# Kernel optimization log

Hardware: AMD Instinct MI355X
Metric: run time of the kernel (lower is better)

## Reference

```python
import jax, jax.numpy as jnp
import numpy as np

EMBED_DIM = 768
MAX_LEN = 1024
ALPHA = 0.99
BATCH = 16


def setup_inputs() -> dict:
    key = jax.random.key(0)
    k1, k2, k3 = jax.random.split(key, 3)
    x = jax.random.normal(k1, (BATCH, MAX_LEN, EMBED_DIM), dtype=jnp.float32)
    # torch nn.Linear(embed_dim, 3*embed_dim): store weight as [in, out] for x @ W
    scale = 1.0 / np.sqrt(EMBED_DIM)
    W_qkv = jax.random.uniform(k2, (EMBED_DIM, 3 * EMBED_DIM), dtype=jnp.float32,
                               minval=-scale, maxval=scale)
    b_qkv = jax.random.uniform(k3, (3 * EMBED_DIM,), dtype=jnp.float32,
                               minval=-scale, maxval=scale)
    return {"x": x, "W_qkv": W_qkv, "b_qkv": b_qkv}


def _retention_mask(sl, alpha, dtype):
    # M[i, j] = alpha**(i - j) if i >= j else 0 (causal tril * decay)
    i = jnp.arange(sl)[:, None]
    j = jnp.arange(sl)[None, :]
    causal = i >= j
    # compute decay only where causal to avoid huge alpha**(negative) values
    exponent = jnp.where(causal, (i - j).astype(dtype), 0.0)
    decay = jnp.asarray(alpha, dtype) ** exponent
    return jnp.where(causal, decay, jnp.zeros((), dtype))


def reference(x, W_qkv, b_qkv):
    bs, sl, d = x.shape
    qkv = x @ W_qkv + b_qkv                      # [B, S, 3D]
    q, k, v = jnp.split(qkv, 3, axis=-1)         # each [B, S, D]
    M = _retention_mask(sl, ALPHA, x.dtype)      # [S, S]
    scores = jnp.einsum('bsd,btd->bst', q, k) / jnp.sqrt(jnp.asarray(d, x.dtype))
    out = jnp.einsum('bst,btd->bsd', scores * M[None, :, :], v)
    return out
```

## Files before the change

### kernel.cpp

```cpp
#include <hip/hip_runtime.h>
#include <hip/hip_bf16.h>


#define SEQ   1024
#define DIM   768
#define ND3   2304

typedef __attribute__((ext_vector_type(8))) short bf16x8;
typedef __attribute__((ext_vector_type(4))) float f32x4;

#define L2A     (-0.014499569695115089f)
#define RSQRTD  (0.03608439182435161f)

__device__ __forceinline__ unsigned short f2bf(float x) {
  union { float f; unsigned u; } v; v.f = x;
  unsigned r = v.u + 0x7FFFu + ((v.u >> 16) & 1u);
  return (unsigned short)(r >> 16);
}

__device__ __forceinline__ void gload16(const void* g, void* l) {
  __builtin_amdgcn_global_load_lds(
      (const __attribute__((address_space(1))) void*)g,
      (__attribute__((address_space(3))) void*)l, 16, 0, 0);
}

__device__ __forceinline__ void gemm256(
    const unsigned short* pA, const unsigned short* pB, int ldA, int ldB,
    char* ls, int nt, int wid, int lane, f32x4 acc[8][4]) {
  int lr = lane & 15, lg = lane >> 4;
  int wm = wid >> 2, wn = wid & 3;
  int slot16 = (((((lr & 1) << 2) | lg) ^ ((lr >> 1) & 7)) << 4);
  int rdA = wm * 8192 + (lr >> 1) * 128 + slot16;
  int rdB = 16384 + wn * 4096 + (lr >> 1) * 128 + slot16;
  int cc = wid * 2;

#define STG(t, half) do {                                                     \
    char* d_ = ls + ((t) & 3) * 32768 + (half) * 16384 + cc * 1024;           \
    const unsigned short* s_ = ((half) ? pB : pA) + (size_t)(t) * 32;         \
    int ld_ = ((half) ? ldB : ldA);                                           \
    gload16(s_ + (size_t)(cc * 16) * ld_, d_);                                \
    gload16(s_ + (size_t)(cc * 16 + 16) * ld_, d_ + 1024);                    \
  } while (0)

  STG(0, 0); STG(0, 1); STG(1, 0); STG(1, 1); STG(2, 0); STG(2, 1);
  asm volatile("s_waitcnt vmcnt(8)" ::: "memory");
  __builtin_amdgcn_s_barrier();
  __builtin_amdgcn_sched_barrier(0);

  for (int t = 0; t < nt; ++t) {
    char* buf = ls + (t & 3) * 32768;
    bf16x8 aF[4], bF[4];
#pragma unroll
    for (int n = 0; n < 4; ++n) bF[n] = *(const bf16x8*)(buf + rdB + n * 1024);
#pragma unroll
    for (int f = 0; f < 4; ++f) aF[f] = *(const bf16x8*)(buf + rdA + f * 1024);
    if (t + 3 < nt) STG(t + 3, 0);
    __builtin_amdgcn_s_setprio(1);
#pragma unroll
    for (int f = 0; f < 4; ++f)
#pragma unroll
      for (int n = 0; n < 4; ++n)
        acc[f][n] = __builtin_amdgcn_mfma_f32_16x16x32_bf16(aF[f], bF[n], acc[f][n], 0, 0, 0);
    __builtin_amdgcn_s_setprio(0);
#pragma unroll
    for (int f = 0; f < 4; ++f) aF[f] = *(const bf16x8*)(buf + rdA + 4096 + f * 1024);
    if (t + 3 < nt) STG(t + 3, 1);
    __builtin_amdgcn_s_setprio(1);
#pragma unroll
    for (int f = 0; f < 4; ++f)
#pragma unroll
      for (int n = 0; n < 4; ++n)
        acc[4 + f][n] = __builtin_amdgcn_mfma_f32_16x16x32_bf16(aF[f], bF[n], acc[4 + f][n], 0, 0, 0);
    __builtin_amdgcn_s_setprio(0);

    if (t == nt - 1) break;
    if (t + 3 < nt)      asm volatile("s_waitcnt vmcnt(8)" ::: "memory");
    else if (t + 2 < nt) asm volatile("s_waitcnt vmcnt(4)" ::: "memory");
    else                 asm volatile("s_waitcnt vmcnt(0)" ::: "memory");
    __builtin_amdgcn_s_barrier();
    __builtin_amdgcn_sched_barrier(0);
  }
#undef STG
}

__global__ void convert_x(const float* __restrict__ x, unsigned short* __restrict__ xb) {
  size_t i = ((size_t)blockIdx.x * 256 + threadIdx.x) * 8;
  float4 f0 = *(const float4*)(x + i);
  float4 f1 = *(const float4*)(x + i + 4);
  bf16x8 v;
  v[0] = (short)f2bf(f0.x); v[1] = (short)f2bf(f0.y);
  v[2] = (short)f2bf(f0.z); v[3] = (short)f2bf(f0.w);
  v[4] = (short)f2bf(f1.x); v[5] = (short)f2bf(f1.y);
  v[6] = (short)f2bf(f1.z); v[7] = (short)f2bf(f1.w);
  *(bf16x8*)(xb + i) = v;
}

__global__ void transpose_w(const float* __restrict__ W, unsigned short* __restrict__ Wt) {
  __shared__ float tile[64][65];
  int n0 = (blockIdx.x % 36) * 64;
  int k0 = (blockIdx.x / 36) * 64;
  int tx = threadIdx.x & 63, ty = threadIdx.x >> 6;
#pragma unroll
  for (int p = 0; p < 16; ++p) {
    int k = ty + p * 4;
    tile[k][tx] = W[(size_t)(k0 + k) * ND3 + n0 + tx];
  }
  __syncthreads();
#pragma unroll
  for (int p = 0; p < 16; ++p) {
    int n = ty + p * 4;
    Wt[(size_t)(n0 + n) * DIM + k0 + tx] = f2bf(tile[tx][n]);
  }
}

__global__ void __launch_bounds__(512, 2) qkv_g8(
    const unsigned short* __restrict__ xb, const unsigned short* __restrict__ Wt,
    const float* __restrict__ bias,
    unsigned short* __restrict__ Qs, unsigned short* __restrict__ Ks,
    unsigned short* __restrict__ Vt) {
  __shared__ char ls[131072];
  int bid = (blockIdx.x & 7) * 72 + (blockIdx.x >> 3);
  int mt = bid / 9, ntb = bid % 9;
  int m0 = mt * 256, n0 = ntb * 256;

  int tid = threadIdx.x, lane = tid & 63, wid = tid >> 6;
  int c8 = (lane & 7) ^ (lane >> 3);
  int rloc = (lane >> 3) * 2 + (c8 >> 2), colo = (c8 & 3) * 8;

  const unsigned short* pA = xb + (size_t)(m0 + rloc) * DIM + colo;
  const unsigned short* pB = Wt + (size_t)(n0 + rloc) * DIM + colo;

  f32x4 acc[8][4] = {};
  gemm256(pA, pB, DIM, DIM, ls, 24, wid, lane, acc);

  int wm = wid >> 2, wn = wid & 3;
  int lr = lane & 15, lg = lane >> 4;
  float bia[4];
#pragma unroll
  for (int n = 0; n < 4; ++n) bia[n] = bias[n0 + wn * 64 + n * 16 + lr];

  if (ntb < 3) {
#pragma unroll
    for (int f = 0; f < 8; ++f)
#pragma unroll
      for (int r = 0; r < 4; ++r) {
        int mg = m0 + wm * 128 + f * 16 + lg * 4 + r;
        int b = mg >> 10, s = mg & 1023;
        float sc = exp2f((float)s * L2A) * RSQRTD;
        unsigned short* dst = Qs + ((size_t)b * SEQ + s) * DIM + n0 + wn * 64 + lr;
#pragma unroll
        for (int n = 0; n < 4; ++n)
          dst[n * 16] = f2bf((acc[f][n][r] + bia[n]) * sc);
      }
  } else if (ntb < 6) {
#pragma unroll
    for (int f = 0; f < 8; ++f)
#pragma unroll
      for (int r = 0; r < 4; ++r) {
        int mg = m0 + wm * 128 + f * 16 + lg * 4 + r;
        int b = mg >> 10, s = mg & 1023;
        float sc = exp2f(-(float)s * L2A);
        unsigned short* dst = Ks + ((size_t)b * SEQ + s) * DIM + (n0 - DIM) + wn * 64 + lr;
#pragma unroll
        for (int n = 0; n < 4; ++n)
          dst[n * 16] = f2bf((acc[f][n][r] + bia[n]) * sc);
      }
  } else {
#pragma unroll
    for (int f = 0; f < 8; ++f)
#pragma unroll
      for (int r = 0; r < 4; ++r) {
        int mg = m0 + wm * 128 + f * 16 + lg * 4 + r;
        int b = mg >> 10, s = mg & 1023;
        int d = (n0 - 2 * DIM) + wn * 64 + lr;
        unsigned short* dst = Vt + ((size_t)b * DIM + d) * SEQ + s;
#pragma unroll
        for (int n = 0; n < 4; ++n)
          dst[(size_t)n * 16 * SEQ] = f2bf(acc[f][n][r] + bia[n]);
      }
  }
}

__global__ void __launch_bounds__(512, 2) score_g8(
    const unsigned short* __restrict__ Qs, const unsigned short* __restrict__ Ks,
    unsigned short* __restrict__ Sm, int b_base) {
  __shared__ char ls[131072];
  const signed char IT[10] = {0,1,1,2,2,2,3,3,3,3};
  const signed char JT[10] = {0,0,1,0,1,2,0,1,2,3};
  int bid = (blockIdx.x & 7) * (gridDim.x >> 3) + (blockIdx.x >> 3);
  int t10 = bid % 10, bl = bid / 10;
  int b = b_base + bl;
  int m0 = IT[t10] * 256, n0 = JT[t10] * 256;
  const unsigned short* A  = Qs + (size_t)b * SEQ * DIM;
  const unsigned short* Bt = Ks + (size_t)b * SEQ * DIM;
  unsigned short* Smp = Sm + (size_t)bl * SEQ * SEQ;

  int tid = threadIdx.x, lane = tid & 63, wid = tid >> 6;
  int c8 = (lane & 7) ^ (lane >> 3);
  int rloc = (lane >> 3) * 2 + (c8 >> 2), colo = (c8 & 3) * 8;

  const unsigned short* pA = A  + (size_t)(m0 + rloc) * DIM + colo;
  const unsigned short* pB = Bt + (size_t)(n0 + rloc) * DIM + colo;

  f32x4 acc[8][4] = {};
  gemm256(pA, pB, DIM, DIM, ls, 24, wid, lane, acc);

  int wm = wid >> 2, wn = wid & 3;
  int lr = lane & 15, lg = lane >> 4;
#pragma unroll
  for (int f = 0; f < 8; ++f)
#pragma unroll
    for (int n = 0; n < 4; ++n) {
      int j = n0 + wn * 64 + n * 16 + lr;
#pragma unroll
      for (int r = 0; r < 4; ++r) {
        int i = m0 + wm * 128 + f * 16 + lg * 4 + r;
        float v = acc[f][n][r];
        if (j > i) v = 0.0f;
        Smp[(size_t)i * SEQ + j] = f2bf(v);
      }
    }
}

__global__ void __launch_bounds__(512, 2) pv_g8(
    const unsigned short* __restrict__ Sm, const unsigned short* __restrict__ Vt,
    float* __restrict__ out, int b_base, int gsz) {
  __shared__ char ls[131072];
  int it = 3 - blockIdx.x / (gsz * 3);
  int rem = blockIdx.x % (gsz * 3);
  int bl = rem / 3, dt = rem % 3;
  int b = b_base + bl;
  int m0 = it * 256, n0 = dt * 256;
  const unsigned short* A  = Sm + (size_t)bl * SEQ * SEQ;
  const unsigned short* Bt = Vt + (size_t)b * DIM * SEQ;
  int nt = (it + 1) * 8;

  int tid = threadIdx.x, lane = tid & 63, wid = tid >> 6;
  int c8 = (lane & 7) ^ (lane >> 3);
  int rloc = (lane >> 3) * 2 + (c8 >> 2), colo = (c8 & 3) * 8;

  const unsigned short* pA = A  + (size_t)(m0 + rloc) * SEQ + colo;
  const unsigned short* pB = Bt + (size_t)(n0 + rloc) * SEQ + colo;

  f32x4 acc[8][4] = {};
  gemm256(pA, pB, SEQ, SEQ, ls, nt, wid, lane, acc);

  int wm = wid >> 2, wn = wid & 3;
  int lr = lane & 15, lg = lane >> 4;
#pragma unroll
  for (int f = 0; f < 8; ++f)
#pragma unroll
    for (int n = 0; n < 4; ++n) {
      int d = n0 + wn * 64 + n * 16 + lr;
#pragma unroll
      for (int r = 0; r < 4; ++r) {
        int i = m0 + wm * 128 + f * 16 + lg * 4 + r;
        out[((size_t)b * SEQ + i) * DIM + d] = acc[f][n][r];
      }
    }
}

extern "C" void kernel_launch(void* const* d_in, const int* in_sizes, int n_in,
                              void* d_out, int out_size, void* d_ws, size_t ws_size,
                              hipStream_t stream) {
  const float* x    = (const float*)d_in[0];
  const float* W    = (const float*)d_in[1];
  const float* bias = (const float*)d_in[2];
  float* out = (float*)d_out;

  char* ws = (char*)d_ws;
  unsigned short* Wt = (unsigned short*)(ws);
  unsigned short* Qs = (unsigned short*)(ws + 3538944);
  unsigned short* Ks = (unsigned short*)(ws + 3538944 + 25165824);
  unsigned short* Vt = (unsigned short*)(ws + 3538944 + 2 * 25165824);
  unsigned short* Sm = (unsigned short*)(ws + 3538944 + 3 * 25165824);
  unsigned short* xb = (unsigned short*)d_out;

  size_t smBase = 3538944 + 3 * (size_t)25165824;
  int gsz = (ws_size >= smBase + (size_t)16 * SEQ * SEQ * 2) ? 16 : 8;
  int ngrp = 16 / gsz;

  transpose_w<<<36 * 12, 256, 0, stream>>>(W, Wt);
  convert_x<<<6144, 256, 0, stream>>>(x, xb);
  qkv_g8<<<576, 512, 0, stream>>>(xb, Wt, bias, Qs, Ks, Vt);
  for (int g = 0; g < ngrp; ++g) {
    score_g8<<<gsz * 10, 512, 0, stream>>>(Qs, Ks, Sm, g * gsz);
    pv_g8<<<gsz * 12, 512, 0, stream>>>(Sm, Vt, out, g * gsz, gsz);
  }
}
```

Before: 157.1 us.

## Shrink GEMM tiles to 128x256 with 4 waves and double-buffered LDS

Replaces the 256x256, 8-wave, 4-stage GEMM core with a 128x256 tile on 4 waves that uses a 2-stage LDS double buffer and two barriers per k-step. Grid sizes double for the qkv, score and pv kernels, and pv gains XCD-aware block swizzling. The two prep kernels are merged into one launch, and the V-transpose epilogue writes 4 contiguous bf16 values per store. The aim is more blocks and better occupancy, with less LDS per block and fewer launches. The cost is less data reuse per tile and a shallower prefetch pipeline.

```diff
diff --git a/kernel.cpp b/kernel.cpp
--- a/kernel.cpp
+++ b/kernel.cpp
@@ -24,130 +24,138 @@
       (__attribute__((address_space(3))) void*)l, 16, 0, 0);
 }
 
-__device__ __forceinline__ void gemm256(
-    const unsigned short* pA, const unsigned short* pB, int ldA, int ldB,
-    char* ls, int nt, int wid, int lane, f32x4 acc[8][4]) {
+__device__ __forceinline__ void gemm_core(
+    const unsigned short* gA, const unsigned short* gB, int ldA, int ldB,
+    char* lsA, char* lsB, int nt, int wid, int lane, f32x4 acc[8][4]) {
   int lr = lane & 15, lg = lane >> 4;
-  int wm = wid >> 2, wn = wid & 3;
-  int slot16 = (((((lr & 1) << 2) | lg) ^ ((lr >> 1) & 7)) << 4);
-  int rdA = wm * 8192 + (lr >> 1) * 128 + slot16;
-  int rdB = 16384 + wn * 4096 + (lr >> 1) * 128 + slot16;
-  int cc = wid * 2;
-
-#define STG(t, half) do {                                                     \
-    char* d_ = ls + ((t) & 3) * 32768 + (half) * 16384 + cc * 1024;           \
-    const unsigned short* s_ = ((half) ? pB : pA) + (size_t)(t) * 32;         \
-    int ld_ = ((half) ? ldB : ldA);                                           \
-    gload16(s_ + (size_t)(cc * 16) * ld_, d_);                                \
-    gload16(s_ + (size_t)(cc * 16 + 16) * ld_, d_ + 1024);                    \
+  int myslot = (((((lr & 1) << 2) | lg) ^ ((lr >> 1) & 7)) << 4);
+  int rdA = (lr >> 1) * 128 + myslot;
+  int rdB = wid * 4096 + (lr >> 1) * 128 + myslot;
+
+#define STAGE(t, par) do {                                                    \
+    char* la_ = lsA + (par) * 8192;                                           \
+    char* lb_ = lsB + (par) * 16384;                                          \
+    const unsigned short* sa_ = gA + (size_t)(t) * 32;                        \
+    const unsigned short* sb_ = gB + (size_t)(t) * 32;                        \
+    gload16(sa_ + (size_t)(wid * 32) * ldA,      la_ + wid * 2048);           \
+    gload16(sa_ + (size_t)(wid * 32 + 16) * ldA, la_ + wid * 2048 + 1024);    \
+    _Pragma("unroll")                                                         \
+    for (int c_ = 0; c_ < 4; ++c_)                                            \
+      gload16(sb_ + (size_t)((wid * 4 + c_) * 16) * ldB,                      \
+              lb_ + (wid * 4 + c_) * 1024);                                   \
   } while (0)
 
-  STG(0, 0); STG(0, 1); STG(1, 0); STG(1, 1); STG(2, 0); STG(2, 1);
-  asm volatile("s_waitcnt vmcnt(8)" ::: "memory");
+  STAGE(0, 0);
+  STAGE(1, 1);
+  asm volatile("s_waitcnt vmcnt(6)" ::: "memory");
   __builtin_amdgcn_s_barrier();
-  __builtin_amdgcn_sched_barrier(0);
+  asm volatile("" ::: "memory");
 
   for (int t = 0; t < nt; ++t) {
-    char* buf = ls + (t & 3) * 32768;
-    bf16x8 aF[4], bF[4];
-#pragma unroll
-    for (int n = 0; n < 4; ++n) bF[n] = *(const bf16x8*)(buf + rdB + n * 1024);
-#pragma unroll
-    for (int f = 0; f < 4; ++f) aF[f] = *(const bf16x8*)(buf + rdA + f * 1024);
-    if (t + 3 < nt) STG(t + 3, 0);
-    __builtin_amdgcn_s_setprio(1);
-#pragma unroll
-    for (int f = 0; f < 4; ++f)
-#pragma unroll
-      for (int n = 0; n < 4; ++n)
-        acc[f][n] = __builtin_amdgcn_mfma_f32_16x16x32_bf16(aF[f], bF[n], acc[f][n], 0, 0, 0);
-    __builtin_amdgcn_s_setprio(0);
-#pragma unroll
-    for (int f = 0; f < 4; ++f) aF[f] = *(const bf16x8*)(buf + rdA + 4096 + f * 1024);
-    if (t + 3 < nt) STG(t + 3, 1);
-    __builtin_amdgcn_s_setprio(1);
-#pragma unroll
-    for (int f = 0; f < 4; ++f)
-#pragma unroll
-      for (int n = 0; n < 4; ++n)
-        acc[4 + f][n] = __builtin_amdgcn_mfma_f32_16x16x32_bf16(aF[f], bF[n], acc[4 + f][n], 0, 0, 0);
-    __builtin_amdgcn_s_setprio(0);
+    int pA = (t & 1) * 8192, pB = (t & 1) * 16384;
+    bf16x8 bF[4];
+#pragma unroll
+    for (int n = 0; n < 4; ++n)
+      bF[n] = *(const bf16x8*)(lsB + pB + rdB + n * 1024);
+#pragma unroll
+    for (int h = 0; h < 2; ++h) {
+      bf16x8 aF[4];
+#pragma unroll
+      for (int f = 0; f < 4; ++f)
+        aF[f] = *(const bf16x8*)(lsA + pA + rdA + (h * 4 + f) * 1024);
+      __builtin_amdgcn_s_setprio(1);
+#pragma unroll
+      for (int f = 0; f < 4; ++f)
+#pragma unroll
+        for (int n = 0; n < 4; ++n)
+          acc[h * 4 + f][n] = __builtin_amdgcn_mfma_f32_16x16x32_bf16(
+              aF[f], bF[n], acc[h * 4 + f][n], 0, 0, 0);
+      __builtin_amdgcn_s_setprio(0);
+    }
 
     if (t == nt - 1) break;
-    if (t + 3 < nt)      asm volatile("s_waitcnt vmcnt(8)" ::: "memory");
-    else if (t + 2 < nt) asm volatile("s_waitcnt vmcnt(4)" ::: "memory");
-    else                 asm volatile("s_waitcnt vmcnt(0)" ::: "memory");
     __builtin_amdgcn_s_barrier();
-    __builtin_amdgcn_sched_barrier(0);
+    asm volatile("" ::: "memory");
+    if (t + 2 < nt) {
+      STAGE(t + 2, t & 1);
+      asm volatile("s_waitcnt vmcnt(6)" ::: "memory");
+    } else {
+      asm volatile("s_waitcnt vmcnt(0)" ::: "memory");
+    }
+    __builtin_amdgcn_s_barrier();
+    asm volatile("" ::: "memory");
   }
-#undef STG
-}
-
-__global__ void convert_x(const float* __restrict__ x, unsigned short* __restrict__ xb) {
-  size_t i = ((size_t)blockIdx.x * 256 + threadIdx.x) * 8;
-  float4 f0 = *(const float4*)(x + i);
-  float4 f1 = *(const float4*)(x + i + 4);
-  bf16x8 v;
-  v[0] = (short)f2bf(f0.x); v[1] = (short)f2bf(f0.y);
-  v[2] = (short)f2bf(f0.z); v[3] = (short)f2bf(f0.w);
-  v[4] = (short)f2bf(f1.x); v[5] = (short)f2bf(f1.y);
-  v[6] = (short)f2bf(f1.z); v[7] = (short)f2bf(f1.w);
-  *(bf16x8*)(xb + i) = v;
-}
-
-__global__ void transpose_w(const float* __restrict__ W, unsigned short* __restrict__ Wt) {
+#undef STAGE
+}
+
+__global__ void prep(const float* __restrict__ x, unsigned short* __restrict__ xb,
+                     const float* __restrict__ W, unsigned short* __restrict__ Wt) {
   __shared__ float tile[64][65];
-  int n0 = (blockIdx.x % 36) * 64;
-  int k0 = (blockIdx.x / 36) * 64;
-  int tx = threadIdx.x & 63, ty = threadIdx.x >> 6;
-#pragma unroll
-  for (int p = 0; p < 16; ++p) {
-    int k = ty + p * 4;
-    tile[k][tx] = W[(size_t)(k0 + k) * ND3 + n0 + tx];
+  int bid = blockIdx.x;
+  if (bid < 6144) {
+    size_t i = ((size_t)bid * 256 + threadIdx.x) * 8;
+    float4 f0 = *(const float4*)(x + i);
+    float4 f1 = *(const float4*)(x + i + 4);
+    bf16x8 v;
+    v[0] = (short)f2bf(f0.x); v[1] = (short)f2bf(f0.y);
+    v[2] = (short)f2bf(f0.z); v[3] = (short)f2bf(f0.w);
+    v[4] = (short)f2bf(f1.x); v[5] = (short)f2bf(f1.y);
+    v[6] = (short)f2bf(f1.z); v[7] = (short)f2bf(f1.w);
+    *(bf16x8*)(xb + i) = v;
+  } else {
+    int tb = bid - 6144;
+    int n0 = (tb % 36) * 64;
+    int k0 = (tb / 36) * 64;
+    int tx = threadIdx.x & 63, ty = threadIdx.x >> 6;
+#pragma unroll
+    for (int p = 0; p < 16; ++p) {
+      int k = ty + p * 4;
+      tile[k][tx] = W[(size_t)(k0 + k) * ND3 + n0 + tx];
+    }
+    __syncthreads();
+#pragma unroll
+    for (int p = 0; p < 16; ++p) {
+      int n = ty + p * 4;
+      Wt[(size_t)(n0 + n) * DIM + k0 + tx] = f2bf(tile[tx][n]);
+    }
   }
-  __syncthreads();
-#pragma unroll
-  for (int p = 0; p < 16; ++p) {
-    int n = ty + p * 4;
-    Wt[(size_t)(n0 + n) * DIM + k0 + tx] = f2bf(tile[tx][n]);
-  }
-}
-
-__global__ void __launch_bounds__(512, 2) qkv_g8(
+}
+
+__global__ void __launch_bounds__(256, 2) qkv_g(
     const unsigned short* __restrict__ xb, const unsigned short* __restrict__ Wt,
     const float* __restrict__ bias,
     unsigned short* __restrict__ Qs, unsigned short* __restrict__ Ks,
     unsigned short* __restrict__ Vt) {
-  __shared__ char ls[131072];
-  int bid = (blockIdx.x & 7) * 72 + (blockIdx.x >> 3);
+  __shared__ __align__(1024) char lsA[16384];
+  __shared__ __align__(1024) char lsB[32768];
+  int bid = (blockIdx.x & 7) * 144 + (blockIdx.x >> 3);
   int mt = bid / 9, ntb = bid % 9;
-  int m0 = mt * 256, n0 = ntb * 256;
+  int m0 = mt * 128, n0 = ntb * 256;
 
   int tid = threadIdx.x, lane = tid & 63, wid = tid >> 6;
   int c8 = (lane & 7) ^ (lane >> 3);
   int rloc = (lane >> 3) * 2 + (c8 >> 2), colo = (c8 & 3) * 8;
 
-  const unsigned short* pA = xb + (size_t)(m0 + rloc) * DIM + colo;
-  const unsigned short* pB = Wt + (size_t)(n0 + rloc) * DIM + colo;
+  const unsigned short* gA = xb + (size_t)(m0 + rloc) * DIM + colo;
+  const unsigned short* gB = Wt + (size_t)(n0 + rloc) * DIM + colo;
 
   f32x4 acc[8][4] = {};
-  gemm256(pA, pB, DIM, DIM, ls, 24, wid, lane, acc);
-
-  int wm = wid >> 2, wn = wid & 3;
+  gemm_core(gA, gB, DIM, DIM, lsA, lsB, 24, wid, lane, acc);
+
   int lr = lane & 15, lg = lane >> 4;
   float bia[4];
 #pragma unroll
-  for (int n = 0; n < 4; ++n) bia[n] = bias[n0 + wn * 64 + n * 16 + lr];
+  for (int n = 0; n < 4; ++n) bia[n] = bias[n0 + wid * 64 + n * 16 + lr];
 
   if (ntb < 3) {
 #pragma unroll
     for (int f = 0; f < 8; ++f)
 #pragma unroll
       for (int r = 0; r < 4; ++r) {
-        int mg = m0 + wm * 128 + f * 16 + lg * 4 + r;
+        int mg = m0 + f * 16 + lg * 4 + r;
         int b = mg >> 10, s = mg & 1023;
         float sc = exp2f((float)s * L2A) * RSQRTD;
-        unsigned short* dst = Qs + ((size_t)b * SEQ + s) * DIM + n0 + wn * 64 + lr;
+        unsigned short* dst = Qs + ((size_t)b * SEQ + s) * DIM + n0 + wid * 64 + lr;
 #pragma unroll
         for (int n = 0; n < 4; ++n)
           dst[n * 16] = f2bf((acc[f][n][r] + bia[n]) * sc);
@@ -157,40 +165,45 @@
     for (int f = 0; f < 8; ++f)
 #pragma unroll
       for (int r = 0; r < 4; ++r) {
-        int mg = m0 + wm * 128 + f * 16 + lg * 4 + r;
+        int mg = m0 + f * 16 + lg * 4 + r;
         int b = mg >> 10, s = mg & 1023;
         float sc = exp2f(-(float)s * L2A);
-        unsigned short* dst = Ks + ((size_t)b * SEQ + s) * DIM + (n0 - DIM) + wn * 64 + lr;
+        unsigned short* dst = Ks + ((size_t)b * SEQ + s) * DIM + (n0 - DIM) + wid * 64 + lr;
 #pragma unroll
         for (int n = 0; n < 4; ++n)
           dst[n * 16] = f2bf((acc[f][n][r] + bia[n]) * sc);
       }
   } else {
 #pragma unroll
-    for (int f = 0; f < 8; ++f)
-#pragma unroll
-      for (int r = 0; r < 4; ++r) {
-        int mg = m0 + wm * 128 + f * 16 + lg * 4 + r;
-        int b = mg >> 10, s = mg & 1023;
-        int d = (n0 - 2 * DIM) + wn * 64 + lr;
-        unsigned short* dst = Vt + ((size_t)b * DIM + d) * SEQ + s;
-#pragma unroll
-        for (int n = 0; n < 4; ++n)
-          dst[(size_t)n * 16 * SEQ] = f2bf(acc[f][n][r] + bia[n]);
-      }
+    for (int f = 0; f < 8; ++f) {
+      int mg = m0 + f * 16 + lg * 4;
+      int b = mg >> 10, s0 = mg & 1023;
+#pragma unroll
+      for (int n = 0; n < 4; ++n) {
+        int d = (n0 - 2 * DIM) + wid * 64 + n * 16 + lr;
+        ushort4 v;
+        v.x = f2bf(acc[f][n][0] + bia[n]);
+        v.y = f2bf(acc[f][n][1] + bia[n]);
+        v.z = f2bf(acc[f][n][2] + bia[n]);
+        v.w = f2bf(acc[f][n][3] + bia[n]);
+        *(ushort4*)(Vt + ((size_t)b * DIM + d) * SEQ + s0) = v;
+      }
+    }
   }
 }
 
-__global__ void __launch_bounds__(512, 2) score_g8(
+__constant__ const signed char IT_TAB[20] = {0,1,2,2,3,3,4,4,4,5,5,5,6,6,6,6,7,7,7,7};
+__constant__ const signed char JT_TAB[20] = {0,0,0,1,0,1,0,1,2,0,1,2,0,1,2,3,0,1,2,3};
+
+__global__ void __launch_bounds__(256, 2) score_g(
     const unsigned short* __restrict__ Qs, const unsigned short* __restrict__ Ks,
     unsigned short* __restrict__ Sm, int b_base) {
-  __shared__ char ls[131072];
-  const signed char IT[10] = {0,1,1,2,2,2,3,3,3,3};
-  const signed char JT[10] = {0,0,1,0,1,2,0,1,2,3};
+  __shared__ __align__(1024) char lsA[16384];
+  __shared__ __align__(1024) char lsB[32768];
   int bid = (blockIdx.x & 7) * (gridDim.x >> 3) + (blockIdx.x >> 3);
-  int t10 = bid % 10, bl = bid / 10;
+  int idx = bid % 20, bl = bid / 20;
   int b = b_base + bl;
-  int m0 = IT[t10] * 256, n0 = JT[t10] * 256;
+  int m0 = IT_TAB[idx] * 128, n0 = JT_TAB[idx] * 256;
   const unsigned short* A  = Qs + (size_t)b * SEQ * DIM;
   const unsigned short* Bt = Ks + (size_t)b * SEQ * DIM;
   unsigned short* Smp = Sm + (size_t)bl * SEQ * SEQ;
@@ -199,22 +212,21 @@
   int c8 = (lane & 7) ^ (lane >> 3);
   int rloc = (lane >> 3) * 2 + (c8 >> 2), colo = (c8 & 3) * 8;
 
-  const unsigned short* pA = A  + (size_t)(m0 + rloc) * DIM + colo;
-  const unsigned short* pB = Bt + (size_t)(n0 + rloc) * DIM + colo;
+  const unsigned short* gA = A  + (size_t)(m0 + rloc) * DIM + colo;
+  const unsigned short* gB = Bt + (size_t)(n0 + rloc) * DIM + colo;
 
   f32x4 acc[8][4] = {};
-  gemm256(pA, pB, DIM, DIM, ls, 24, wid, lane, acc);
-
-  int wm = wid >> 2, wn = wid & 3;
+  gemm_core(gA, gB, DIM, DIM, lsA, lsB, 24, wid, lane, acc);
+
   int lr = lane & 15, lg = lane >> 4;
 #pragma unroll
   for (int f = 0; f < 8; ++f)
 #pragma unroll
     for (int n = 0; n < 4; ++n) {
-      int j = n0 + wn * 64 + n * 16 + lr;
+      int j = n0 + wid * 64 + n * 16 + lr;
 #pragma unroll
       for (int r = 0; r < 4; ++r) {
-        int i = m0 + wm * 128 + f * 16 + lg * 4 + r;
+        int i = m0 + f * 16 + lg * 4 + r;
         float v = acc[f][n][r];
         if (j > i) v = 0.0f;
         Smp[(size_t)i * SEQ + j] = f2bf(v);
@@ -222,39 +234,40 @@
     }
 }
 
-__global__ void __launch_bounds__(512, 2) pv_g8(
+__global__ void __launch_bounds__(256, 2) pv_g(
     const unsigned short* __restrict__ Sm, const unsigned short* __restrict__ Vt,
     float* __restrict__ out, int b_base, int gsz) {
-  __shared__ char ls[131072];
-  int it = 3 - blockIdx.x / (gsz * 3);
-  int rem = blockIdx.x % (gsz * 3);
+  __shared__ __align__(1024) char lsA[16384];
+  __shared__ __align__(1024) char lsB[32768];
+  int bid = (blockIdx.x & 7) * (gridDim.x >> 3) + (blockIdx.x >> 3);
+  int it = 7 - bid / (gsz * 3);
+  int rem = bid % (gsz * 3);
   int bl = rem / 3, dt = rem % 3;
   int b = b_base + bl;
-  int m0 = it * 256, n0 = dt * 256;
+  int m0 = it * 128, n0 = dt * 256;
   const unsigned short* A  = Sm + (size_t)bl * SEQ * SEQ;
   const unsigned short* Bt = Vt + (size_t)b * DIM * SEQ;
-  int nt = (it + 1) * 8;
+  int nt = (it + 1) * 4;
 
   int tid = threadIdx.x, lane = tid & 63, wid = tid >> 6;
   int c8 = (lane & 7) ^ (lane >> 3);
   int rloc = (lane >> 3) * 2 + (c8 >> 2), colo = (c8 & 3) * 8;
 
-  const unsigned short* pA = A  + (size_t)(m0 + rloc) * SEQ + colo;
-  const unsigned short* pB = Bt + (size_t)(n0 + rloc) * SEQ + colo;
+  const unsigned short* gA = A  + (size_t)(m0 + rloc) * SEQ + colo;
+  const unsigned short* gB = Bt + (size_t)(n0 + rloc) * SEQ + colo;
 
   f32x4 acc[8][4] = {};
-  gemm256(pA, pB, SEQ, SEQ, ls, nt, wid, lane, acc);
-
-  int wm = wid >> 2, wn = wid & 3;
+  gemm_core(gA, gB, SEQ, SEQ, lsA, lsB, nt, wid, lane, acc);
+
   int lr = lane & 15, lg = lane >> 4;
 #pragma unroll
   for (int f = 0; f < 8; ++f)
 #pragma unroll
     for (int n = 0; n < 4; ++n) {
-      int d = n0 + wn * 64 + n * 16 + lr;
+      int d = n0 + wid * 64 + n * 16 + lr;
 #pragma unroll
       for (int r = 0; r < 4; ++r) {
-        int i = m0 + wm * 128 + f * 16 + lg * 4 + r;
+        int i = m0 + f * 16 + lg * 4 + r;
         out[((size_t)b * SEQ + i) * DIM + d] = acc[f][n][r];
       }
     }
@@ -280,11 +293,10 @@
   int gsz = (ws_size >= smBase + (size_t)16 * SEQ * SEQ * 2) ? 16 : 8;
   int ngrp = 16 / gsz;
 
-  transpose_w<<<36 * 12, 256, 0, stream>>>(W, Wt);
-  convert_x<<<6144, 256, 0, stream>>>(x, xb);
-  qkv_g8<<<576, 512, 0, stream>>>(xb, Wt, bias, Qs, Ks, Vt);
+  prep<<<6576, 256, 0, stream>>>(x, xb, W, Wt);
+  qkv_g<<<1152, 256, 0, stream>>>(xb, Wt, bias, Qs, Ks, Vt);
   for (int g = 0; g < ngrp; ++g) {
-    score_g8<<<gsz * 10, 512, 0, stream>>>(Qs, Ks, Sm, g * gsz);
-    pv_g8<<<gsz * 12, 512, 0, stream>>>(Sm, Vt, out, g * gsz, gsz);
+    score_g<<<gsz * 20, 256, 0, stream>>>(Qs, Ks, Sm, g * gsz);
+    pv_g<<<gsz * 24, 256, 0, stream>>>(Sm, Vt, out, g * gsz, gsz);
   }
 }
```

Result: slower. 176.0 us (+12.1%).
